# Optimization experiments

Measured on AMD Instinct MI355X. Metric: run time of the kernel, lower is better.

## Reference

```python
import jax, jax.numpy as jnp
import numpy as np

INPUT_DIM = 1024
DAY_EMB = 8
PRED_LEN = 96
HIDDEN = 512
BATCH = 4096


def setup_inputs() -> dict:
    key = jax.random.key(0)
    ks = jax.random.split(key, 6)
    x = jax.random.normal(ks[0], (BATCH, INPUT_DIM), dtype=jnp.float32)
    day_emb = jax.random.normal(ks[1], (PRED_LEN, DAY_EMB), dtype=jnp.float32)
    # stacked per-head first-layer weights: in = input_dim + day_emb_dim
    W1 = jax.random.normal(ks[2], (PRED_LEN, INPUT_DIM + DAY_EMB, HIDDEN), dtype=jnp.float32) * 0.02
    b1 = jax.random.normal(ks[3], (PRED_LEN, HIDDEN), dtype=jnp.float32) * 0.02
    # stacked per-head output Linear(hidden, 1) weights (squeezed)
    W2 = jax.random.normal(ks[4], (PRED_LEN, HIDDEN), dtype=jnp.float32) * 0.02
    b2 = jax.random.normal(ks[5], (PRED_LEN,), dtype=jnp.float32) * 0.02
    return {"x": x, "day_emb": day_emb, "W1": W1, "b1": b1, "W2": W2, "b2": b2}


def reference(x, day_emb, W1, b1, W2, b2):
    # Each head p sees f = concat([x, day_emb[p]]) -> Linear -> ReLU -> (Dropout eval=id) -> Linear(.,1)
    # Split W1 into the x-part and emb-part so we never materialize the [P,B,in+emb] concat.
    W1x = W1[:, :INPUT_DIM, :]          # [P, D, H]
    W1e = W1[:, INPUT_DIM:, :]          # [P, E, H]
    h = jnp.einsum('bd,pdh->pbh', x, W1x)  # [P, B, H]
    h = h + (jnp.einsum('pe,peh->ph', day_emb, W1e) + b1)[:, None, :]
    h = jax.nn.relu(h)
    out = jnp.einsum('pbh,ph->pb', h, W2) + b2[:, None]  # [P, B]
    return out.T  # [B, pred_len]
```

## Files before the change

kernel.cpp:

```cpp
#include <hip/hip_runtime.h>
#include <hip/hip_bf16.h>
#include <stdint.h>

#define INPUT_DIM 1024
#define PRED_LEN 96
#define HIDDEN 512
#define BATCH 4096
#define W1_ROWS 1032

typedef __attribute__((ext_vector_type(8))) short bf16x8;
typedef __attribute__((ext_vector_type(4))) float floatx4;

__device__ __forceinline__ unsigned short f32_to_bf16_rne(float f) {
    union { float f; unsigned int u; } v; v.f = f;
    unsigned int u = v.u;
    unsigned int r = u + 0x7fffu + ((u >> 16) & 1u);
    return (unsigned short)(r >> 16);
}

__device__ __forceinline__ void async_copy16(const void* g, void* l) {
    __builtin_amdgcn_global_load_lds(
        (const __attribute__((address_space(1))) unsigned int*)g,
        (__attribute__((address_space(3))) unsigned int*)l, 16, 0, 0);
}

__global__ void convert_x_kernel(const float* __restrict__ x,
                                 unsigned short* __restrict__ xb) {
    int i = (blockIdx.x * 256 + threadIdx.x) * 4;
    float4 v = *reinterpret_cast<const float4*>(x + i);
    ushort4 o;
    o.x = f32_to_bf16_rne(v.x);
    o.y = f32_to_bf16_rne(v.y);
    o.z = f32_to_bf16_rne(v.z);
    o.w = f32_to_bf16_rne(v.w);
    *reinterpret_cast<ushort4*>(xb + i) = o;
}

__global__ void transpose_w1_kernel(const float* __restrict__ W1,
                                    unsigned short* __restrict__ W1t) {
    __shared__ unsigned short tile[64 * 64];
    int bid = blockIdx.x;
    int nt = bid & 7;
    int kt = (bid >> 3) & 15;
    int p  = bid >> 7;
    int t  = threadIdx.x;
    const float* src = W1 + (size_t)p * W1_ROWS * HIDDEN;
    const int k0 = kt * 64, n0 = nt * 64;

    const int tn = t & 15;
    const int tk = t >> 4;
    float4 v[4];
    #pragma unroll
    for (int i = 0; i < 4; ++i)
        v[i] = *reinterpret_cast<const float4*>(src + (size_t)(k0 + 4 * tk + i) * HIDDEN + n0 + 4 * tn);
    const int slot1 = ((tk >> 2) ^ (tn & 3)) * 16 + (tk & 3) * 4;
    {
        ushort4 w0, w1, w2, w3;
        w0.x = f32_to_bf16_rne(v[0].x); w0.y = f32_to_bf16_rne(v[1].x);
        w0.z = f32_to_bf16_rne(v[2].x); w0.w = f32_to_bf16_rne(v[3].x);
        w1.x = f32_to_bf16_rne(v[0].y); w1.y = f32_to_bf16_rne(v[1].y);
        w1.z = f32_to_bf16_rne(v[2].y); w1.w = f32_to_bf16_rne(v[3].y);
        w2.x = f32_to_bf16_rne(v[0].z); w2.y = f32_to_bf16_rne(v[1].z);
        w2.z = f32_to_bf16_rne(v[2].z); w2.w = f32_to_bf16_rne(v[3].z);
        w3.x = f32_to_bf16_rne(v[0].w); w3.y = f32_to_bf16_rne(v[1].w);
        w3.z = f32_to_bf16_rne(v[2].w); w3.w = f32_to_bf16_rne(v[3].w);
        *reinterpret_cast<ushort4*>(tile + (4 * tn + 0) * 64 + slot1) = w0;
        *reinterpret_cast<ushort4*>(tile + (4 * tn + 1) * 64 + slot1) = w1;
        *reinterpret_cast<ushort4*>(tile + (4 * tn + 2) * 64 + slot1) = w2;
        *reinterpret_cast<ushort4*>(tile + (4 * tn + 3) * 64 + slot1) = w3;
    }
    __syncthreads();

    const int nr = t >> 2;
    const int q  = t & 3;
    const int slot2 = (q ^ ((nr >> 2) & 3)) * 16;
    uint4 a = *reinterpret_cast<const uint4*>(tile + nr * 64 + slot2);
    uint4 b = *reinterpret_cast<const uint4*>(tile + nr * 64 + slot2 + 8);
    size_t dst = ((size_t)p * HIDDEN + n0 + nr) * 1024 + k0 + q * 16;
    *reinterpret_cast<uint4*>(W1t + dst)     = a;
    *reinterpret_cast<uint4*>(W1t + dst + 8) = b;
}

__global__ void bias_kernel(const float* __restrict__ W1,
                            const float* __restrict__ day_emb,
                            const float* __restrict__ b1,
                            float* __restrict__ bias) {
    int p = blockIdx.x;
    int h = threadIdx.x;
    const float* W1e = W1 + ((size_t)p * W1_ROWS + INPUT_DIM) * HIDDEN;
    float acc = b1[p * HIDDEN + h];
    #pragma unroll
    for (int e = 0; e < 8; ++e)
        acc += day_emb[p * 8 + e] * W1e[(size_t)e * HIDDEN + h];
    bias[p * HIDDEN + h] = acc;
}

__global__ void __launch_bounds__(256, 3)
mlp_head_kernel(const unsigned short* __restrict__ xb,
                const unsigned short* __restrict__ W1t,
                const float* __restrict__ bias,
                const float* __restrict__ W2,
                const float* __restrict__ b2,
                float* __restrict__ out)
{
    __shared__ unsigned short As[128 * 64];
    __shared__ unsigned short Bs[128 * 64];
    __shared__ float w2s[HIDDEN];
    __shared__ float biass[HIDDEN];
    __shared__ float red[2][128];

    const int mt   = blockIdx.x;
    const int p    = blockIdx.y;
    const int t    = threadIdx.x;
    const int lane = t & 63;
    const int w    = t >> 6;
    const int wi   = w >> 1;
    const int wj   = w & 1;
    const int l15  = lane & 15;
    const int quad = lane >> 4;
    const int xl   = l15 & 7;

    const int t3    = t >> 3;
    const int skc   = ((t & 7) ^ (t3 & 7)) * 8;
    const int ldsq8 = t * 8;

    for (int i = t; i < HIDDEN; i += 256) {
        w2s[i]   = W2[p * HIDDEN + i];
        biass[i] = bias[p * HIDDEN + i];
    }

    const int m0 = mt * 128;
    const unsigned short* ag = xb  + (size_t)m0 * 1024 + (size_t)t3 * 1024 + skc;
    const unsigned short* bg = W1t + (size_t)p * HIDDEN * 1024 + (size_t)t3 * 1024 + skc;

    float partial[4][4];
    #pragma unroll
    for (int i = 0; i < 4; ++i)
        #pragma unroll
        for (int r = 0; r < 4; ++r) partial[i][r] = 0.f;

    for (int nt = 0; nt < 4; ++nt) {
        floatx4 acc[4][4];
        #pragma unroll
        for (int i = 0; i < 4; ++i)
            #pragma unroll
            for (int j = 0; j < 4; ++j)
                acc[i][j] = (floatx4){0.f, 0.f, 0.f, 0.f};

        const size_t bn = (size_t)nt * 128 * 1024;

        for (int k0 = 0; k0 < 1024; k0 += 64) {
            __syncthreads();
            #pragma unroll
            for (int c = 0; c < 4; ++c) {
                async_copy16(ag + (size_t)c * 32 * 1024 + k0,      As + ldsq8 + c * 2048);
                async_copy16(bg + bn + (size_t)c * 32 * 1024 + k0, Bs + ldsq8 + c * 2048);
            }
            __syncthreads();
            #pragma unroll
            for (int kk = 0; kk < 2; ++kk) {
                const int slot = (kk * 4 + quad) ^ xl;
                bf16x8 af[4], bfr[4];
                #pragma unroll
                for (int i = 0; i < 4; ++i) {
                    int r = wi * 64 + i * 16 + l15;
                    af[i] = *reinterpret_cast<const bf16x8*>(As + r * 64 + slot * 8);
                }
                #pragma unroll
                for (int j = 0; j < 4; ++j) {
                    int n = wj * 64 + j * 16 + l15;
                    bfr[j] = *reinterpret_cast<const bf16x8*>(Bs + n * 64 + slot * 8);
                }
                #pragma unroll
                for (int i = 0; i < 4; ++i)
                    #pragma unroll
                    for (int j = 0; j < 4; ++j)
                        acc[i][j] = __builtin_amdgcn_mfma_f32_16x16x32_bf16(
                            af[i], bfr[j], acc[i][j], 0, 0, 0);
            }
        }

        const int n0 = nt * 128;
        #pragma unroll
        for (int j = 0; j < 4; ++j) {
            int c = n0 + wj * 64 + j * 16 + l15;
            float w2v = w2s[c];
            float bv  = biass[c];
            #pragma unroll
            for (int i = 0; i < 4; ++i)
                #pragma unroll
                for (int r = 0; r < 4; ++r) {
                    float hv = acc[i][j][r] + bv;
                    hv = hv > 0.f ? hv : 0.f;
                    partial[i][r] += hv * w2v;
                }
        }
    }

    #pragma unroll
    for (int i = 0; i < 4; ++i)
        #pragma unroll
        for (int r = 0; r < 4; ++r) {
            float v = partial[i][r];
            v += __shfl_xor(v, 1);
            v += __shfl_xor(v, 2);
            v += __shfl_xor(v, 4);
            v += __shfl_xor(v, 8);
            partial[i][r] = v;
        }

    if (l15 == 0) {
        #pragma unroll
        for (int i = 0; i < 4; ++i)
            #pragma unroll
            for (int r = 0; r < 4; ++r) {
                int row = wi * 64 + i * 16 + quad * 4 + r;
                red[wj][row] = partial[i][r];
            }
    }
    __syncthreads();
    if (t < 128) {
        float v = red[0][t] + red[1][t] + b2[p];
        out[(size_t)(m0 + t) * PRED_LEN + p] = v;
    }
}

extern "C" void kernel_launch(void* const* d_in, const int* in_sizes, int n_in,
                              void* d_out, int out_size, void* d_ws, size_t ws_size,
                              hipStream_t stream) {
    const float* x       = (const float*)d_in[0];
    const float* day_emb = (const float*)d_in[1];
    const float* W1      = (const float*)d_in[2];
    const float* b1      = (const float*)d_in[3];
    const float* W2      = (const float*)d_in[4];
    const float* b2      = (const float*)d_in[5];
    float* out = (float*)d_out;

    const size_t xb_bytes  = (size_t)BATCH * INPUT_DIM * 2;
    const size_t w1t_bytes = (size_t)PRED_LEN * HIDDEN * INPUT_DIM * 2;
    const size_t bias_bytes = (size_t)PRED_LEN * HIDDEN * 4;
    if (ws_size < xb_bytes + w1t_bytes + bias_bytes) return;

    unsigned short* xb  = (unsigned short*)d_ws;
    unsigned short* w1t = (unsigned short*)((char*)d_ws + xb_bytes);
    float* biasp        = (float*)((char*)d_ws + xb_bytes + w1t_bytes);

    convert_x_kernel<<<(BATCH * INPUT_DIM) / (256 * 4), 256, 0, stream>>>(x, xb);
    transpose_w1_kernel<<<PRED_LEN * 16 * 8, 256, 0, stream>>>(W1, w1t);
    bias_kernel<<<PRED_LEN, HIDDEN, 0, stream>>>(W1, day_emb, b1, biasp);

    dim3 grid(BATCH / 128, PRED_LEN);
    mlp_head_kernel<<<grid, 256, 0, stream>>>(xb, w1t, biasp, W2, b2, out);
}
```

Measured before the change: 676.4 us.

## Read A fragments directly from global using a pre-blocked x layout

The x conversion kernel now writes bf16 x in a tiled layout matching MFMA fragment order, and the GEMM kernel loads A fragments directly from global memory instead of staging them through shared memory. This removes half the LDS traffic and async copies and frees LDS for occupancy. The cost is exposing global/L2 latency on the A operand inside the inner loop, with A reloaded redundantly across waves and N tiles.

```diff
diff --git a/kernel.cpp b/kernel.cpp
--- a/kernel.cpp
+++ b/kernel.cpp
@@ -25,15 +25,20 @@
 }
 
 __global__ void convert_x_kernel(const float* __restrict__ x,
-                                 unsigned short* __restrict__ xb) {
-    int i = (blockIdx.x * 256 + threadIdx.x) * 4;
-    float4 v = *reinterpret_cast<const float4*>(x + i);
+                                 unsigned short* __restrict__ xa) {
+    int g = (blockIdx.x * 256 + threadIdx.x) * 4;
+    float4 v = *reinterpret_cast<const float4*>(x + g);
     ushort4 o;
     o.x = f32_to_bf16_rne(v.x);
     o.y = f32_to_bf16_rne(v.y);
     o.z = f32_to_bf16_rne(v.z);
     o.w = f32_to_bf16_rne(v.w);
-    *reinterpret_cast<ushort4*>(xb + i) = o;
+    int mg = g >> 10;
+    int k  = g & 1023;
+    int mt = mg >> 7, m = mg & 127;
+    int kt = k >> 6, kk = (k >> 5) & 1, ke = k & 31;
+    size_t idx = (size_t)mt * 131072 + (kt * 2 + kk) * 4096 + m * 32 + ke;
+    *reinterpret_cast<ushort4*>(xa + idx) = o;
 }
 
 __global__ void transpose_w1_kernel(const float* __restrict__ W1,
@@ -96,14 +101,13 @@
 }
 
 __global__ void __launch_bounds__(256, 3)
-mlp_head_kernel(const unsigned short* __restrict__ xb,
+mlp_head_kernel(const unsigned short* __restrict__ xa,
                 const unsigned short* __restrict__ W1t,
                 const float* __restrict__ bias,
                 const float* __restrict__ W2,
                 const float* __restrict__ b2,
                 float* __restrict__ out)
 {
-    __shared__ unsigned short As[128 * 64];
     __shared__ unsigned short Bs[128 * 64];
     __shared__ float w2s[HIDDEN];
     __shared__ float biass[HIDDEN];
@@ -130,8 +134,10 @@
     }
 
     const int m0 = mt * 128;
-    const unsigned short* ag = xb  + (size_t)m0 * 1024 + (size_t)t3 * 1024 + skc;
-    const unsigned short* bg = W1t + (size_t)p * HIDDEN * 1024 + (size_t)t3 * 1024 + skc;
+    const unsigned short* pA = xa + (size_t)mt * 131072
+                              + (wi * 64 + l15) * 32 + quad * 8;
+    const unsigned short* bg = W1t + (size_t)p * HIDDEN * 1024
+                              + (size_t)t3 * 1024 + skc;
 
     float partial[4][4];
     #pragma unroll
@@ -152,20 +158,18 @@
         for (int k0 = 0; k0 < 1024; k0 += 64) {
             __syncthreads();
             #pragma unroll
-            for (int c = 0; c < 4; ++c) {
-                async_copy16(ag + (size_t)c * 32 * 1024 + k0,      As + ldsq8 + c * 2048);
+            for (int c = 0; c < 4; ++c)
                 async_copy16(bg + bn + (size_t)c * 32 * 1024 + k0, Bs + ldsq8 + c * 2048);
-            }
             __syncthreads();
+            const int ktk = (k0 >> 6) * 2;
             #pragma unroll
             for (int kk = 0; kk < 2; ++kk) {
                 const int slot = (kk * 4 + quad) ^ xl;
+                const unsigned short* pAk = pA + (size_t)(ktk + kk) * 4096;
                 bf16x8 af[4], bfr[4];
                 #pragma unroll
-                for (int i = 0; i < 4; ++i) {
-                    int r = wi * 64 + i * 16 + l15;
-                    af[i] = *reinterpret_cast<const bf16x8*>(As + r * 64 + slot * 8);
-                }
+                for (int i = 0; i < 4; ++i)
+                    af[i] = *reinterpret_cast<const bf16x8*>(pAk + i * 512);
                 #pragma unroll
                 for (int j = 0; j < 4; ++j) {
                     int n = wj * 64 + j * 16 + l15;
@@ -236,19 +240,19 @@
     const float* b2      = (const float*)d_in[5];
     float* out = (float*)d_out;
 
-    const size_t xb_bytes  = (size_t)BATCH * INPUT_DIM * 2;
+    const size_t xa_bytes  = (size_t)BATCH * INPUT_DIM * 2;
     const size_t w1t_bytes = (size_t)PRED_LEN * HIDDEN * INPUT_DIM * 2;
     const size_t bias_bytes = (size_t)PRED_LEN * HIDDEN * 4;
-    if (ws_size < xb_bytes + w1t_bytes + bias_bytes) return;
-
-    unsigned short* xb  = (unsigned short*)d_ws;
-    unsigned short* w1t = (unsigned short*)((char*)d_ws + xb_bytes);
-    float* biasp        = (float*)((char*)d_ws + xb_bytes + w1t_bytes);
-
-    convert_x_kernel<<<(BATCH * INPUT_DIM) / (256 * 4), 256, 0, stream>>>(x, xb);
+    if (ws_size < xa_bytes + w1t_bytes + bias_bytes) return;
+
+    unsigned short* xa  = (unsigned short*)d_ws;
+    unsigned short* w1t = (unsigned short*)((char*)d_ws + xa_bytes);
+    float* biasp        = (float*)((char*)d_ws + xa_bytes + w1t_bytes);
+
+    convert_x_kernel<<<(BATCH * INPUT_DIM) / (256 * 4), 256, 0, stream>>>(x, xa);
     transpose_w1_kernel<<<PRED_LEN * 16 * 8, 256, 0, stream>>>(W1, w1t);
     bias_kernel<<<PRED_LEN, HIDDEN, 0, stream>>>(W1, day_emb, b1, biasp);
 
     dim3 grid(BATCH / 128, PRED_LEN);
-    mlp_head_kernel<<<grid, 256, 0, stream>>>(xb, w1t, biasp, W2, b2, out);
-}
+    mlp_head_kernel<<<grid, 256, 0, stream>>>(xa, w1t, biasp, W2, b2, out);
+}
```

Measured after the change: 944.6 us. 1.4x slower.
